# Performance work log

Measured on AMD Instinct MI355X. Metric: run time of the kernel, lower is better.

## Reference

```python
import jax, jax.numpy as jnp
import numpy as np

EPS = 1e-5
SLOPE = 0.1
R = 7  # num_relation

def _bn(x, g, b):
    # BatchNorm1d in training mode: per-feature batch mean / biased variance
    m = jnp.mean(x, axis=0)
    v = jnp.var(x, axis=0)
    return (x - m) * jax.lax.rsqrt(v + EPS) * g + b

def _lrelu(x):
    return jnp.where(x >= 0, x, SLOPE * x)

def setup_inputs() -> dict:
    key = jax.random.key(0)
    ks = jax.random.split(key, 10)
    N, E, D, DE = 50000, 800000, 128, 64
    h_v = jax.random.normal(ks[0], (N, D), dtype=jnp.float32)
    node_in = jax.random.randint(ks[1], (E,), 0, N)
    node_out = jax.random.randint(ks[2], (E,), 0, N)
    relation_type = jax.random.randint(ks[3], (E,), 0, R)
    h_e = jax.random.normal(ks[4], (E, DE), dtype=jnp.float32)
    s = 0.02
    return {
        "h_v": h_v, "node_in": node_in, "node_out": node_out,
        "relation_type": relation_type, "h_e": h_e,
        # input MLP: BN -> LReLU -> Linear(D,D,bias) -> BN -> LReLU
        "in_bn1_g": jnp.ones((D,)), "in_bn1_b": jnp.zeros((D,)),
        "in_W": jax.random.normal(ks[5], (D, D), dtype=jnp.float32) * s,
        "in_b": jnp.zeros((D,)),
        "in_bn2_g": jnp.ones((D,)), "in_bn2_b": jnp.zeros((D,)),
        # edge MLP: BN -> LReLU -> Linear(DE,D,bias) -> BN -> LReLU
        "e_bn1_g": jnp.ones((DE,)), "e_bn1_b": jnp.zeros((DE,)),
        "e_W": jax.random.normal(ks[6], (DE, D), dtype=jnp.float32) * s,
        "e_b": jnp.zeros((D,)),
        "e_bn2_g": jnp.ones((D,)), "e_bn2_b": jnp.zeros((D,)),
        # linear: BN(R*D) -> LReLU -> Linear(R*D, D, no bias)
        "lin_bn_g": jnp.ones((R * D,)), "lin_bn_b": jnp.zeros((R * D,)),
        "lin_W": jax.random.normal(ks[7], (R * D, D), dtype=jnp.float32) * s,
        # output: BN(D) -> LReLU -> Linear(D, D, no bias)
        "out_bn_g": jnp.ones((D,)), "out_bn_b": jnp.zeros((D,)),
        "out_W": jax.random.normal(ks[8], (D, D), dtype=jnp.float32) * s,
    }

def reference(h_v, node_in, node_out, relation_type, h_e,
              in_bn1_g, in_bn1_b, in_W, in_b, in_bn2_g, in_bn2_b,
              e_bn1_g, e_bn1_b, e_W, e_b, e_bn2_g, e_bn2_b,
              lin_bn_g, lin_bn_b, lin_W, out_bn_g, out_bn_b, out_W):
    N, D = h_v.shape
    identity = h_v  # input_dim == output_dim -> identity branch is passthrough
    # self.input MLP
    x = _lrelu(_bn(h_v, in_bn1_g, in_bn1_b))
    x = x @ in_W + in_b
    x = _lrelu(_bn(x, in_bn2_g, in_bn2_b))
    # gather + edge MLP add
    msg = x[node_in]  # [E, D]
    e = _lrelu(_bn(h_e, e_bn1_g, e_bn1_b))
    e = e @ e_W + e_b
    e = _lrelu(_bn(e, e_bn2_g, e_bn2_b))
    msg = msg + e
    # relation-indexed scatter_sum
    seg = node_out * R + relation_type  # [E]
    update = jax.ops.segment_sum(msg, seg, num_segments=N * R)  # [N*R, D]
    update = update.reshape(N, R * D)
    # self.linear
    out = _lrelu(_bn(update, lin_bn_g, lin_bn_b)) @ lin_W
    # self.output + residual
    out = _lrelu(_bn(out, out_bn_g, out_bn_b)) @ out_W + identity
    return out
```

## Files before the change

kernel.cpp:

```cpp
#include <hip/hip_runtime.h>

#define EPS 1e-5f
#define SLOPE 0.1f
#define DIM 128
#define DE 64
#define RNUM 7
#define RD (RNUM * DIM)
#define NPB 4

__device__ __forceinline__ float lrelu(float x) { return x >= 0.f ? x : SLOPE * x; }
__device__ __forceinline__ void atomAddF(float* p, float v) { unsafeAtomicAdd(p, v); }

template<int F, int BLK>
__global__ void colstats(const float* __restrict__ x, int nrows, float* __restrict__ out) {
  constexpr int G = BLK / F;
  int f = threadIdx.x % F;
  int g = threadIdx.x / F;
  float s = 0.f, q = 0.f;
  for (int r = blockIdx.x * G + g; r < nrows; r += gridDim.x * G) {
    float v = x[(size_t)r * F + f];
    s += v; q += v * v;
  }
  if constexpr (G > 1) {
    __shared__ float ls[BLK], lq[BLK];
    ls[threadIdx.x] = s; lq[threadIdx.x] = q;
    __syncthreads();
    if (g == 0) {
      #pragma unroll
      for (int i = 1; i < G; i++) { s += ls[i * F + f]; q += lq[i * F + f]; }
    }
  }
  if (g == 0) { atomAddF(&out[f], s); atomAddF(&out[F + f], q); }
}

template<bool HAS_BIAS, bool RESID, bool STATS>
__global__ __launch_bounds__(128) void mlp128(
    const float* __restrict__ xin, const float* __restrict__ W,
    const float* __restrict__ bias,
    const float* __restrict__ bng, const float* __restrict__ bnb,
    const float* __restrict__ stats_in, float invN, int N,
    const float* __restrict__ resid,
    float* __restrict__ out, float* __restrict__ stats_out) {
  __shared__ float tile[32 * DIM];
  int t = threadIdx.x;
  float a, c;
  {
    float mean = stats_in[t] * invN;
    float var = stats_in[DIM + t] * invN - mean * mean;
    a = bng[t] * rsqrtf(var + EPS);
    c = bnb[t] - mean * a;
  }
  int r0 = blockIdx.x * 32;
  int nr = min(32, N - r0);
  for (int r = 0; r < 32; r++) {
    float v = 0.f;
    if (r < nr) {
      v = xin[(size_t)(r0 + r) * DIM + t];
      v = lrelu(v * a + c);
    }
    tile[r * DIM + t] = v;
  }
  __syncthreads();
  int cg = t & 31, rg = t >> 5;
  float acc[8][4];
  #pragma unroll
  for (int rr = 0; rr < 8; rr++) { acc[rr][0]=0.f; acc[rr][1]=0.f; acc[rr][2]=0.f; acc[rr][3]=0.f; }
  const float4* W4 = (const float4*)W;
  #pragma unroll 2
  for (int k = 0; k < DIM; k += 4) {
    float4 w0 = W4[(k + 0) * 32 + cg];
    float4 w1 = W4[(k + 1) * 32 + cg];
    float4 w2 = W4[(k + 2) * 32 + cg];
    float4 w3 = W4[(k + 3) * 32 + cg];
    #pragma unroll
    for (int rr = 0; rr < 8; rr++) {
      float4 tv = *(const float4*)&tile[(rg * 8 + rr) * DIM + k];
      acc[rr][0] += tv.x * w0.x + tv.y * w1.x + tv.z * w2.x + tv.w * w3.x;
      acc[rr][1] += tv.x * w0.y + tv.y * w1.y + tv.z * w2.y + tv.w * w3.y;
      acc[rr][2] += tv.x * w0.z + tv.y * w1.z + tv.z * w2.z + tv.w * w3.z;
      acc[rr][3] += tv.x * w0.w + tv.y * w1.w + tv.z * w2.w + tv.w * w3.w;
    }
  }
  float4 bv = make_float4(0.f, 0.f, 0.f, 0.f);
  if (HAS_BIAS) bv = ((const float4*)bias)[cg];
  float s0=0,s1=0,s2=0,s3=0,q0=0,q1=0,q2=0,q3=0;
  #pragma unroll
  for (int rr = 0; rr < 8; rr++) {
    int r = rg * 8 + rr;
    if (r < nr) {
      float o0 = acc[rr][0] + bv.x;
      float o1 = acc[rr][1] + bv.y;
      float o2 = acc[rr][2] + bv.z;
      float o3 = acc[rr][3] + bv.w;
      if (RESID) {
        const float4 rv = *(const float4*)&resid[(size_t)(r0 + r) * DIM + cg * 4];
        o0 += rv.x; o1 += rv.y; o2 += rv.z; o3 += rv.w;
      }
      *(float4*)&out[(size_t)(r0 + r) * DIM + cg * 4] = make_float4(o0, o1, o2, o3);
      if (STATS) {
        s0 += o0; q0 += o0 * o0; s1 += o1; q1 += o1 * o1;
        s2 += o2; q2 += o2 * o2; s3 += o3; q3 += o3 * o3;
      }
    }
  }
  if (STATS) {
    __syncthreads();
    float* reds = tile;
    float* redq = tile + 512;
    int col = cg * 4;
    reds[rg * DIM + col + 0] = s0; reds[rg * DIM + col + 1] = s1;
    reds[rg * DIM + col + 2] = s2; reds[rg * DIM + col + 3] = s3;
    redq[rg * DIM + col + 0] = q0; redq[rg * DIM + col + 1] = q1;
    redq[rg * DIM + col + 2] = q2; redq[rg * DIM + col + 3] = q3;
    __syncthreads();
    if (rg == 0) {
      #pragma unroll
      for (int cc = 0; cc < 4; cc++) {
        int cl = col + cc;
        float ss = reds[cl] + reds[DIM + cl] + reds[2 * DIM + cl] + reds[3 * DIM + cl];
        float qq = redq[cl] + redq[DIM + cl] + redq[2 * DIM + cl] + redq[3 * DIM + cl];
        atomAddF(&stats_out[cl], ss);
        atomAddF(&stats_out[DIM + cl], qq);
      }
    }
  }
}

__global__ __launch_bounds__(256) void x2k(float* __restrict__ x1,
    const float* __restrict__ s_x1, const float* __restrict__ g,
    const float* __restrict__ b, float invN, int total4) {
  int i = blockIdx.x * 256 + threadIdx.x;
  if (i >= total4) return;
  int col = (i & 31) * 4;
  float4 v = ((float4*)x1)[i];
  float m0 = s_x1[col + 0] * invN, m1 = s_x1[col + 1] * invN;
  float m2 = s_x1[col + 2] * invN, m3 = s_x1[col + 3] * invN;
  float a0 = g[col + 0] * rsqrtf(s_x1[DIM + col + 0] * invN - m0 * m0 + EPS);
  float a1 = g[col + 1] * rsqrtf(s_x1[DIM + col + 1] * invN - m1 * m1 + EPS);
  float a2 = g[col + 2] * rsqrtf(s_x1[DIM + col + 2] * invN - m2 * m2 + EPS);
  float a3 = g[col + 3] * rsqrtf(s_x1[DIM + col + 3] * invN - m3 * m3 + EPS);
  v.x = lrelu(v.x * a0 + (b[col + 0] - m0 * a0));
  v.y = lrelu(v.y * a1 + (b[col + 1] - m1 * a1));
  v.z = lrelu(v.z * a2 + (b[col + 2] - m2 * a2));
  v.w = lrelu(v.w * a3 + (b[col + 3] - m3 * a3));
  ((float4*)x1)[i] = v;
}

__global__ __launch_bounds__(128) void lin_mlp(
    const float* __restrict__ upd, const float* __restrict__ W,
    const float* __restrict__ bng, const float* __restrict__ bnb,
    const float* __restrict__ stats_in, float invN, int N,
    float* __restrict__ out, float* __restrict__ stats_out) {
  __shared__ float tile[32 * DIM];
  int t = threadIdx.x;
  int r0 = blockIdx.x * 32;
  int nr = min(32, N - r0);
  int cg = t & 31, rg = t >> 5;
  float acc[8][4];
  #pragma unroll
  for (int rr = 0; rr < 8; rr++) { acc[rr][0]=0.f; acc[rr][1]=0.f; acc[rr][2]=0.f; acc[rr][3]=0.f; }
  const float4* W4 = (const float4*)W;
  for (int kt = 0; kt < RNUM; kt++) {
    int cb = kt * DIM;
    float a, c;
    {
      int col = cb + t;
      float mean = stats_in[col] * invN;
      float var = stats_in[RD + col] * invN - mean * mean;
      a = bng[col] * rsqrtf(var + EPS);
      c = bnb[col] - mean * a;
    }
    for (int r = 0; r < 32; r++) {
      float v = 0.f;
      if (r < nr) {
        v = upd[(size_t)(r0 + r) * RD + cb + t];
        v = lrelu(v * a + c);
      }
      tile[r * DIM + t] = v;
    }
    __syncthreads();
    #pragma unroll 2
    for (int k = 0; k < DIM; k += 4) {
      float4 w0 = W4[(cb + k + 0) * 32 + cg];
      float4 w1 = W4[(cb + k + 1) * 32 + cg];
      float4 w2 = W4[(cb + k + 2) * 32 + cg];
      float4 w3 = W4[(cb + k + 3) * 32 + cg];
      #pragma unroll
      for (int rr = 0; rr < 8; rr++) {
        float4 tv = *(const float4*)&tile[(rg * 8 + rr) * DIM + k];
        acc[rr][0] += tv.x * w0.x + tv.y * w1.x + tv.z * w2.x + tv.w * w3.x;
        acc[rr][1] += tv.x * w0.y + tv.y * w1.y + tv.z * w2.y + tv.w * w3.y;
        acc[rr][2] += tv.x * w0.z + tv.y * w1.z + tv.z * w2.z + tv.w * w3.z;
        acc[rr][3] += tv.x * w0.w + tv.y * w1.w + tv.z * w2.w + tv.w * w3.w;
      }
    }
    __syncthreads();
  }
  float s0=0,s1=0,s2=0,s3=0,q0=0,q1=0,q2=0,q3=0;
  #pragma unroll
  for (int rr = 0; rr < 8; rr++) {
    int r = rg * 8 + rr;
    if (r < nr) {
      float o0 = acc[rr][0], o1 = acc[rr][1], o2 = acc[rr][2], o3 = acc[rr][3];
      *(float4*)&out[(size_t)(r0 + r) * DIM + cg * 4] = make_float4(o0, o1, o2, o3);
      s0 += o0; q0 += o0 * o0; s1 += o1; q1 += o1 * o1;
      s2 += o2; q2 += o2 * o2; s3 += o3; q3 += o3 * o3;
    }
  }
  __syncthreads();
  float* reds = tile;
  float* redq = tile + 512;
  int col = cg * 4;
  reds[rg * DIM + col + 0] = s0; reds[rg * DIM + col + 1] = s1;
  reds[rg * DIM + col + 2] = s2; reds[rg * DIM + col + 3] = s3;
  redq[rg * DIM + col + 0] = q0; redq[rg * DIM + col + 1] = q1;
  redq[rg * DIM + col + 2] = q2; redq[rg * DIM + col + 3] = q3;
  __syncthreads();
  if (rg == 0) {
    #pragma unroll
    for (int cc = 0; cc < 4; cc++) {
      int cl = col + cc;
      float ss = reds[cl] + reds[DIM + cl] + reds[2 * DIM + cl] + reds[3 * DIM + cl];
      float qq = redq[cl] + redq[DIM + cl] + redq[2 * DIM + cl] + redq[3 * DIM + cl];
      atomAddF(&stats_out[cl], ss);
      atomAddF(&stats_out[DIM + cl], qq);
    }
  }
}

__global__ __launch_bounds__(256) void gram_kernel(
    const float* __restrict__ he, int E,
    const float* __restrict__ g1, const float* __restrict__ b1,
    const float* __restrict__ s_he, float invE,
    float* __restrict__ parts, int tilesPerBlock) {
  __shared__ float yt[32 * DE];
  int t = threadIdx.x;
  int f = t & 63;
  float a, c;
  {
    float mean = s_he[f] * invE;
    float var = s_he[DE + f] * invE - mean * mean;
    a = g1[f] * rsqrtf(var + EPS);
    c = b1[f] - mean * a;
  }
  int k1b = t >> 4, k2b = t & 15;
  float accG[4][4];
  #pragma unroll
  for (int i = 0; i < 4; i++) { accG[i][0]=0.f; accG[i][1]=0.f; accG[i][2]=0.f; accG[i][3]=0.f; }
  float colsum = 0.f;
  long long tile0 = (long long)blockIdx.x * tilesPerBlock;
  for (int tt = 0; tt < tilesPerBlock; tt++) {
    int e0 = (int)((tile0 + tt) * 32);
    if (e0 >= E) break;
    __syncthreads();
    #pragma unroll
    for (int i = 0; i < 8; i++) {
      int r = (t + i * 256) >> 6;
      int e = e0 + r;
      float v = 0.f;
      if (e < E) v = lrelu(he[(size_t)e * DE + f] * a + c);
      yt[r * DE + f] = v;
      colsum += v;
    }
    __syncthreads();
    #pragma unroll 4
    for (int r = 0; r < 32; r++) {
      float4 ya = *(const float4*)&yt[r * DE + k1b * 4];
      float4 yb = *(const float4*)&yt[r * DE + k2b * 4];
      accG[0][0] += ya.x * yb.x; accG[0][1] += ya.x * yb.y; accG[0][2] += ya.x * yb.z; accG[0][3] += ya.x * yb.w;
      accG[1][0] += ya.y * yb.x; accG[1][1] += ya.y * yb.y; accG[1][2] += ya.y * yb.z; accG[1][3] += ya.y * yb.w;
      accG[2][0] += ya.z * yb.x; accG[2][1] += ya.z * yb.y; accG[2][2] += ya.z * yb.z; accG[2][3] += ya.z * yb.w;
      accG[3][0] += ya.w * yb.x; accG[3][1] += ya.w * yb.y; accG[3][2] += ya.w * yb.z; accG[3][3] += ya.w * yb.w;
    }
  }
  __syncthreads();
  yt[t] = colsum;
  __syncthreads();
  float* outp = parts + (size_t)blockIdx.x * 4160;
  #pragma unroll
  for (int i = 0; i < 4; i++)
    #pragma unroll
    for (int j = 0; j < 4; j++)
      outp[(k1b * 4 + i) * DE + k2b * 4 + j] = accG[i][j];
  if (t < DE) outp[4096 + t] = yt[t] + yt[t + 64] + yt[t + 128] + yt[t + 192];
}

__global__ __launch_bounds__(256) void gram_reduce(const float* __restrict__ parts, int P,
    float* __restrict__ gram, float* __restrict__ gcol) {
  int j = blockIdx.x * 256 + threadIdx.x;
  if (j >= 4160) return;
  float s = 0.f;
  for (int p = 0; p < P; p++) s += parts[(size_t)p * 4160 + j];
  if (j < 4096) gram[j] = s; else gcol[j - 4096] = s;
}

__global__ __launch_bounds__(128) void ebn2_partial(
    const float* __restrict__ gram, const float* __restrict__ gcol,
    const float* __restrict__ eW, float invE,
    float* __restrict__ q, float* __restrict__ m1) {
  int j = threadIdx.x;
  int k1 = blockIdx.x;
  float wk1 = eW[k1 * DIM + j];
  float s = 0.f;
  for (int k2 = 0; k2 < DE; k2++) s += eW[k2 * DIM + j] * gram[k1 * DE + k2];
  atomAddF(&q[j], wk1 * s * invE);
  if (k1 == 0) {
    float m = 0.f;
    for (int k = 0; k < DE; k++) m += gcol[k] * eW[k * DIM + j];
    m1[j] = m * invE;
  }
}

__global__ void count_k(const int* __restrict__ nout, int E, int* __restrict__ cnt) {
  for (int e = blockIdx.x * blockDim.x + threadIdx.x; e < E; e += gridDim.x * blockDim.x)
    atomicAdd(&cnt[nout[e]], 1);
}

__global__ __launch_bounds__(256) void scan1(const int* __restrict__ in, int n,
    int* __restrict__ excl, int* __restrict__ sums) {
  __shared__ int s[256];
  int i = blockIdx.x * 256 + threadIdx.x;
  int v = (i < n) ? in[i] : 0;
  s[threadIdx.x] = v; __syncthreads();
  for (int off = 1; off < 256; off <<= 1) {
    int x = (threadIdx.x >= off) ? s[threadIdx.x - off] : 0;
    __syncthreads(); s[threadIdx.x] += x; __syncthreads();
  }
  if (i < n) excl[i] = s[threadIdx.x] - v;
  if (threadIdx.x == 255) sums[blockIdx.x] = s[255];
}

__global__ __launch_bounds__(1024) void scan2(int* __restrict__ sums, int nch) {
  __shared__ int s[1024];
  int t = threadIdx.x;
  int v = (t < nch) ? sums[t] : 0;
  s[t] = v; __syncthreads();
  for (int off = 1; off < 1024; off <<= 1) {
    int x = (t >= off) ? s[t - off] : 0;
    __syncthreads(); s[t] += x; __syncthreads();
  }
  if (t < nch) sums[t] = s[t] - v;
}

__global__ __launch_bounds__(256) void scan3(const int* __restrict__ excl,
    const int* __restrict__ sums, int n, int E,
    int* __restrict__ base, int* __restrict__ cursor) {
  int i = blockIdx.x * 256 + threadIdx.x;
  if (i < n) { int b = excl[i] + sums[blockIdx.x]; base[i] = b; cursor[i] = b; }
  if (i == 0) base[n] = E;
}

__global__ void scatter_k(const int* __restrict__ nout, const int* __restrict__ nin,
    const int* __restrict__ rel, int E, int* __restrict__ cursor, int2* __restrict__ elist2) {
  for (int e = blockIdx.x * blockDim.x + threadIdx.x; e < E; e += gridDim.x * blockDim.x) {
    int n = nout[e];
    int pos = atomicAdd(&cursor[n], 1);
    elist2[pos] = make_int2(e, (nin[e] << 3) | rel[e]);
  }
}

__global__ __launch_bounds__(128) void fused_edge_scatter(
    const float* __restrict__ he, const int2* __restrict__ elist2,
    const int* __restrict__ base, const float* __restrict__ eW,
    const float* __restrict__ eg1, const float* __restrict__ eb1,
    const float* __restrict__ s_he, float invE,
    const float* __restrict__ qv, const float* __restrict__ m1v,
    const float* __restrict__ eg2, const float* __restrict__ eb2,
    const float* __restrict__ x2, int N, float* __restrict__ upd) {
  __shared__ float accs[NPB * RD];
  __shared__ float yt[32 * DE];
  __shared__ float a2s[DIM], c2s[DIM];
  __shared__ int s_eid[32], s_nl[32], s_gr[32];
  int t = threadIdx.x;
  int n0 = blockIdx.x * NPB;
  int f = t & 63;
  float ae1, ce1;
  {
    float me = s_he[f] * invE;
    float ve = s_he[DE + f] * invE - me * me;
    ae1 = eg1[f] * rsqrtf(ve + EPS);
    ce1 = eb1[f] - me * ae1;
  }
  {
    float m = m1v[t];
    float a = eg2[t] * rsqrtf(qv[t] - m * m + EPS);
    a2s[t] = a;
    c2s[t] = eb2[t] - m * a;
  }
  for (int i = t; i < NPB * RD; i += 128) accs[i] = 0.f;
  int estart = base[n0];
  int eend = base[min(n0 + NPB, N)];
  int bb1 = base[min(n0 + 1, N)];
  int bb2 = base[min(n0 + 2, N)];
  int bb3 = base[min(n0 + 3, N)];
  __syncthreads();
  int cg = t & 31, rg = t >> 5;
  const float4* W4 = (const float4*)eW;
  for (int e0 = estart; e0 < eend; e0 += 32) {
    if (t < 32) {
      int pos = e0 + t;
      int2 ee = (pos < eend) ? elist2[pos] : make_int2(0, 0);
      s_eid[t] = ee.x;
      s_gr[t] = ee.y;
      s_nl[t] = (pos >= bb3) ? 3 : (pos >= bb2) ? 2 : (pos >= bb1) ? 1 : 0;
    }
    __syncthreads();
    #pragma unroll
    for (int i = 0; i < 16; i++) {
      int r = (t + i * 128) >> 6;
      float v = 0.f;
      if (e0 + r < eend) v = lrelu(he[(size_t)s_eid[r] * DE + f] * ae1 + ce1);
      yt[r * DE + f] = v;
    }
    __syncthreads();
    float a8[8][4];
    #pragma unroll
    for (int rr = 0; rr < 8; rr++) { a8[rr][0]=0.f; a8[rr][1]=0.f; a8[rr][2]=0.f; a8[rr][3]=0.f; }
    #pragma unroll 2
    for (int k = 0; k < DE; k += 4) {
      float4 w0 = W4[(k + 0) * 32 + cg];
      float4 w1 = W4[(k + 1) * 32 + cg];
      float4 w2 = W4[(k + 2) * 32 + cg];
      float4 w3 = W4[(k + 3) * 32 + cg];
      #pragma unroll
      for (int rr = 0; rr < 8; rr++) {
        float4 tv = *(const float4*)&yt[(rg * 8 + rr) * DE + k];
        a8[rr][0] += tv.x * w0.x + tv.y * w1.x + tv.z * w2.x + tv.w * w3.x;
        a8[rr][1] += tv.x * w0.y + tv.y * w1.y + tv.z * w2.y + tv.w * w3.y;
        a8[rr][2] += tv.x * w0.z + tv.y * w1.z + tv.z * w2.z + tv.w * w3.z;
        a8[rr][3] += tv.x * w0.w + tv.y * w1.w + tv.z * w2.w + tv.w * w3.w;
      }
    }
    float4 a2 = *(const float4*)&a2s[cg * 4];
    float4 c2 = *(const float4*)&c2s[cg * 4];
    int aoff[8];
    #pragma unroll
    for (int rr = 0; rr < 8; rr++) {
      int r = rg * 8 + rr;
      if (e0 + r < eend) {
        int gr = s_gr[r];
        const float4 xv = *(const float4*)&x2[(size_t)(gr >> 3) * DIM + cg * 4];
        a8[rr][0] = lrelu(a8[rr][0] * a2.x + c2.x) + xv.x;
        a8[rr][1] = lrelu(a8[rr][1] * a2.y + c2.y) + xv.y;
        a8[rr][2] = lrelu(a8[rr][2] * a2.z + c2.z) + xv.z;
        a8[rr][3] = lrelu(a8[rr][3] * a2.w + c2.w) + xv.w;
        aoff[rr] = s_nl[r] * RD + (gr & 7) * DIM + cg * 4;
      } else aoff[rr] = -1;
    }
    #pragma unroll
    for (int p = 0; p < 4; p++) {
      if (rg == p) {
        #pragma unroll
        for (int rr = 0; rr < 8; rr++) {
          int o = aoff[rr];
          if (o >= 0) {
            accs[o + 0] += a8[rr][0];
            accs[o + 1] += a8[rr][1];
            accs[o + 2] += a8[rr][2];
            accs[o + 3] += a8[rr][3];
          }
        }
      }
      __syncthreads();
    }
  }
  int nn = min(NPB, N - n0);
  for (int i = t; i < nn * RD; i += 128)
    upd[(size_t)n0 * RD + i] = accs[i];
}

extern "C" void kernel_launch(void* const* d_in, const int* in_sizes, int n_in,
                              void* d_out, int out_size, void* d_ws, size_t ws_size,
                              hipStream_t stream) {
  const float* h_v      = (const float*)d_in[0];
  const int*   node_in  = (const int*)d_in[1];
  const int*   node_out = (const int*)d_in[2];
  const int*   rel      = (const int*)d_in[3];
  const float* h_e      = (const float*)d_in[4];
  const float* in_bn1_g = (const float*)d_in[5];
  const float* in_bn1_b = (const float*)d_in[6];
  const float* in_W     = (const float*)d_in[7];
  const float* in_b     = (const float*)d_in[8];
  const float* in_bn2_g = (const float*)d_in[9];
  const float* in_bn2_b = (const float*)d_in[10];
  const float* e_bn1_g  = (const float*)d_in[11];
  const float* e_bn1_b  = (const float*)d_in[12];
  const float* e_W      = (const float*)d_in[13];
  const float* e_bn2_g  = (const float*)d_in[15];
  const float* e_bn2_b  = (const float*)d_in[16];
  const float* lin_bn_g = (const float*)d_in[17];
  const float* lin_bn_b = (const float*)d_in[18];
  const float* lin_W    = (const float*)d_in[19];
  const float* out_bn_g = (const float*)d_in[20];
  const float* out_bn_b = (const float*)d_in[21];
  const float* out_W    = (const float*)d_in[22];

  int N = in_sizes[0] / DIM;
  int E = in_sizes[1];
  if (N <= 0 || E <= 0) return;
  float invN = 1.f / (float)N;
  float invE = 1.f / (float)E;

  float* ws   = (float*)d_ws;
  float* upd  = ws;
  float* x1   = upd + (size_t)N * RD;
  float* stats = x1 + (size_t)N * DIM;
  float* s_hv = stats;
  float* s_x1 = s_hv + 2 * DIM;
  float* s_he = s_x1 + 2 * DIM;
  float* qv   = s_he + 2 * DE;
  float* m1v  = qv + DIM;
  float* s_up = m1v + DIM;
  float* s_o1 = s_up + 2 * RD;
  float* gram = s_o1 + 2 * DIM;
  float* gcol = gram + DE * DE;
  float* statsEnd = gcol + DE;
  size_t statsFloats = (size_t)(statsEnd - stats);
  int2* elist2 = (int2*)statsEnd;
  int* cnt    = (int*)(elist2 + E);
  int* sums   = cnt + N;
  int* base   = sums + 1024;
  int* cursor = base + N + 1;
  float* parts = upd;

  int nBlk32 = (N + 31) / 32;
  int nch = (N + 255) / 256;

  hipMemsetAsync(stats, 0, statsFloats * sizeof(float), stream);
  hipMemsetAsync(cnt, 0, (size_t)N * sizeof(int), stream);

  colstats<DIM, 256><<<512, 256, 0, stream>>>(h_v, N, s_hv);
  mlp128<true, false, true><<<nBlk32, 128, 0, stream>>>(
      h_v, in_W, in_b, in_bn1_g, in_bn1_b, s_hv, invN, N, nullptr, x1, s_x1);
  x2k<<<(N * 32 + 255) / 256, 256, 0, stream>>>(x1, s_x1, in_bn2_g, in_bn2_b, invN, N * 32);

  colstats<DE, 256><<<1024, 256, 0, stream>>>(h_e, E, s_he);

  count_k<<<1024, 256, 0, stream>>>(node_out, E, cnt);
  scan1<<<nch, 256, 0, stream>>>(cnt, N, cnt, sums);
  scan2<<<1, 1024, 0, stream>>>(sums, nch);
  scan3<<<nch, 256, 0, stream>>>(cnt, sums, N, E, base, cursor);
  scatter_k<<<1024, 256, 0, stream>>>(node_out, node_in, rel, E, cursor, elist2);

  {
    int tiles = 32;
    int P = (E + 32 * tiles - 1) / (32 * tiles);
    gram_kernel<<<P, 256, 0, stream>>>(h_e, E, e_bn1_g, e_bn1_b, s_he, invE, parts, tiles);
    gram_reduce<<<(4160 + 255) / 256, 256, 0, stream>>>(parts, P, gram, gcol);
  }
  ebn2_partial<<<DE, 128, 0, stream>>>(gram, gcol, e_W, invE, qv, m1v);

  fused_edge_scatter<<<(N + NPB - 1) / NPB, 128, 0, stream>>>(
      h_e, elist2, base, e_W, e_bn1_g, e_bn1_b, s_he, invE,
      qv, m1v, e_bn2_g, e_bn2_b, x1, N, upd);

  colstats<RD, RD><<<448, RD, 0, stream>>>(upd, N, s_up);
  lin_mlp<<<nBlk32, 128, 0, stream>>>(upd, lin_W, lin_bn_g, lin_bn_b, s_up, invN, N,
                                      x1, s_o1);
  mlp128<false, true, false><<<nBlk32, 128, 0, stream>>>(
      x1, out_W, nullptr, out_bn_g, out_bn_b, s_o1, invN, N, h_v, (float*)d_out, nullptr);
}
```

Measured before the change: 2.099 ms.

## Retile GEMM kernels to 4x8 register blocks and fold input BN into edge scatter

```diff
diff --git a/kernel.cpp b/kernel.cpp
--- a/kernel.cpp
+++ b/kernel.cpp
@@ -7,6 +7,8 @@
 #define RNUM 7
 #define RD (RNUM * DIM)
 #define NPB 4
+#define TP 132
+#define YP 68
 
 __device__ __forceinline__ float lrelu(float x) { return x >= 0.f ? x : SLOPE * x; }
 __device__ __forceinline__ void atomAddF(float* p, float v) { unsafeAtomicAdd(p, v); }
@@ -41,7 +43,7 @@
     const float* __restrict__ stats_in, float invN, int N,
     const float* __restrict__ resid,
     float* __restrict__ out, float* __restrict__ stats_out) {
-  __shared__ float tile[32 * DIM];
+  __shared__ float tile[32 * TP];
   int t = threadIdx.x;
   float a, c;
   {
@@ -58,92 +60,86 @@
       v = xin[(size_t)(r0 + r) * DIM + t];
       v = lrelu(v * a + c);
     }
-    tile[r * DIM + t] = v;
+    tile[r * TP + t] = v;
   }
   __syncthreads();
-  int cg = t & 31, rg = t >> 5;
-  float acc[8][4];
-  #pragma unroll
-  for (int rr = 0; rr < 8; rr++) { acc[rr][0]=0.f; acc[rr][1]=0.f; acc[rr][2]=0.f; acc[rr][3]=0.f; }
+  int cg = t & 15, rg = t >> 4;
+  int c0 = cg * 8;
+  float acc[4][8];
+  #pragma unroll
+  for (int rr = 0; rr < 4; rr++)
+    #pragma unroll
+    for (int j = 0; j < 8; j++) acc[rr][j] = 0.f;
   const float4* W4 = (const float4*)W;
   #pragma unroll 2
   for (int k = 0; k < DIM; k += 4) {
-    float4 w0 = W4[(k + 0) * 32 + cg];
-    float4 w1 = W4[(k + 1) * 32 + cg];
-    float4 w2 = W4[(k + 2) * 32 + cg];
-    float4 w3 = W4[(k + 3) * 32 + cg];
-    #pragma unroll
-    for (int rr = 0; rr < 8; rr++) {
-      float4 tv = *(const float4*)&tile[(rg * 8 + rr) * DIM + k];
-      acc[rr][0] += tv.x * w0.x + tv.y * w1.x + tv.z * w2.x + tv.w * w3.x;
-      acc[rr][1] += tv.x * w0.y + tv.y * w1.y + tv.z * w2.y + tv.w * w3.y;
-      acc[rr][2] += tv.x * w0.z + tv.y * w1.z + tv.z * w2.z + tv.w * w3.z;
-      acc[rr][3] += tv.x * w0.w + tv.y * w1.w + tv.z * w2.w + tv.w * w3.w;
-    }
-  }
-  float4 bv = make_float4(0.f, 0.f, 0.f, 0.f);
-  if (HAS_BIAS) bv = ((const float4*)bias)[cg];
-  float s0=0,s1=0,s2=0,s3=0,q0=0,q1=0,q2=0,q3=0;
-  #pragma unroll
-  for (int rr = 0; rr < 8; rr++) {
-    int r = rg * 8 + rr;
+    float4 wa0 = W4[(k + 0) * 32 + cg * 2], wb0 = W4[(k + 0) * 32 + cg * 2 + 1];
+    float4 wa1 = W4[(k + 1) * 32 + cg * 2], wb1 = W4[(k + 1) * 32 + cg * 2 + 1];
+    float4 wa2 = W4[(k + 2) * 32 + cg * 2], wb2 = W4[(k + 2) * 32 + cg * 2 + 1];
+    float4 wa3 = W4[(k + 3) * 32 + cg * 2], wb3 = W4[(k + 3) * 32 + cg * 2 + 1];
+    #pragma unroll
+    for (int rr = 0; rr < 4; rr++) {
+      float4 tv = *(const float4*)&tile[(rg * 4 + rr) * TP + k];
+      acc[rr][0] += tv.x * wa0.x + tv.y * wa1.x + tv.z * wa2.x + tv.w * wa3.x;
+      acc[rr][1] += tv.x * wa0.y + tv.y * wa1.y + tv.z * wa2.y + tv.w * wa3.y;
+      acc[rr][2] += tv.x * wa0.z + tv.y * wa1.z + tv.z * wa2.z + tv.w * wa3.z;
+      acc[rr][3] += tv.x * wa0.w + tv.y * wa1.w + tv.z * wa2.w + tv.w * wa3.w;
+      acc[rr][4] += tv.x * wb0.x + tv.y * wb1.x + tv.z * wb2.x + tv.w * wb3.x;
+      acc[rr][5] += tv.x * wb0.y + tv.y * wb1.y + tv.z * wb2.y + tv.w * wb3.y;
+      acc[rr][6] += tv.x * wb0.z + tv.y * wb1.z + tv.z * wb2.z + tv.w * wb3.z;
+      acc[rr][7] += tv.x * wb0.w + tv.y * wb1.w + tv.z * wb2.w + tv.w * wb3.w;
+    }
+  }
+  float bv[8];
+  #pragma unroll
+  for (int j = 0; j < 8; j++) bv[j] = 0.f;
+  if (HAS_BIAS) {
+    float4 ba = ((const float4*)bias)[cg * 2], bb = ((const float4*)bias)[cg * 2 + 1];
+    bv[0]=ba.x; bv[1]=ba.y; bv[2]=ba.z; bv[3]=ba.w; bv[4]=bb.x; bv[5]=bb.y; bv[6]=bb.z; bv[7]=bb.w;
+  }
+  float s[8], q[8];
+  #pragma unroll
+  for (int j = 0; j < 8; j++) { s[j] = 0.f; q[j] = 0.f; }
+  #pragma unroll
+  for (int rr = 0; rr < 4; rr++) {
+    int r = rg * 4 + rr;
     if (r < nr) {
-      float o0 = acc[rr][0] + bv.x;
-      float o1 = acc[rr][1] + bv.y;
-      float o2 = acc[rr][2] + bv.z;
-      float o3 = acc[rr][3] + bv.w;
+      float o[8];
+      #pragma unroll
+      for (int j = 0; j < 8; j++) o[j] = acc[rr][j] + bv[j];
       if (RESID) {
-        const float4 rv = *(const float4*)&resid[(size_t)(r0 + r) * DIM + cg * 4];
-        o0 += rv.x; o1 += rv.y; o2 += rv.z; o3 += rv.w;
-      }
-      *(float4*)&out[(size_t)(r0 + r) * DIM + cg * 4] = make_float4(o0, o1, o2, o3);
+        float4 ra = *(const float4*)&resid[(size_t)(r0 + r) * DIM + c0];
+        float4 rb = *(const float4*)&resid[(size_t)(r0 + r) * DIM + c0 + 4];
+        o[0]+=ra.x; o[1]+=ra.y; o[2]+=ra.z; o[3]+=ra.w;
+        o[4]+=rb.x; o[5]+=rb.y; o[6]+=rb.z; o[7]+=rb.w;
+      }
+      *(float4*)&out[(size_t)(r0 + r) * DIM + c0]     = make_float4(o[0], o[1], o[2], o[3]);
+      *(float4*)&out[(size_t)(r0 + r) * DIM + c0 + 4] = make_float4(o[4], o[5], o[6], o[7]);
       if (STATS) {
-        s0 += o0; q0 += o0 * o0; s1 += o1; q1 += o1 * o1;
-        s2 += o2; q2 += o2 * o2; s3 += o3; q3 += o3 * o3;
+        #pragma unroll
+        for (int j = 0; j < 8; j++) { s[j] += o[j]; q[j] += o[j] * o[j]; }
       }
     }
   }
   if (STATS) {
     __syncthreads();
     float* reds = tile;
-    float* redq = tile + 512;
-    int col = cg * 4;
-    reds[rg * DIM + col + 0] = s0; reds[rg * DIM + col + 1] = s1;
-    reds[rg * DIM + col + 2] = s2; reds[rg * DIM + col + 3] = s3;
-    redq[rg * DIM + col + 0] = q0; redq[rg * DIM + col + 1] = q1;
-    redq[rg * DIM + col + 2] = q2; redq[rg * DIM + col + 3] = q3;
+    float* redq = tile + 1024;
+    #pragma unroll
+    for (int j = 0; j < 8; j++) { reds[rg * DIM + c0 + j] = s[j]; redq[rg * DIM + c0 + j] = q[j]; }
     __syncthreads();
     if (rg == 0) {
       #pragma unroll
-      for (int cc = 0; cc < 4; cc++) {
-        int cl = col + cc;
-        float ss = reds[cl] + reds[DIM + cl] + reds[2 * DIM + cl] + reds[3 * DIM + cl];
-        float qq = redq[cl] + redq[DIM + cl] + redq[2 * DIM + cl] + redq[3 * DIM + cl];
+      for (int j = 0; j < 8; j++) {
+        int cl = c0 + j;
+        float ss = 0.f, qq = 0.f;
+        #pragma unroll
+        for (int g = 0; g < 8; g++) { ss += reds[g * DIM + cl]; qq += redq[g * DIM + cl]; }
         atomAddF(&stats_out[cl], ss);
         atomAddF(&stats_out[DIM + cl], qq);
       }
     }
   }
-}
-
-__global__ __launch_bounds__(256) void x2k(float* __restrict__ x1,
-    const float* __restrict__ s_x1, const float* __restrict__ g,
-    const float* __restrict__ b, float invN, int total4) {
-  int i = blockIdx.x * 256 + threadIdx.x;
-  if (i >= total4) return;
-  int col = (i & 31) * 4;
-  float4 v = ((float4*)x1)[i];
-  float m0 = s_x1[col + 0] * invN, m1 = s_x1[col + 1] * invN;
-  float m2 = s_x1[col + 2] * invN, m3 = s_x1[col + 3] * invN;
-  float a0 = g[col + 0] * rsqrtf(s_x1[DIM + col + 0] * invN - m0 * m0 + EPS);
-  float a1 = g[col + 1] * rsqrtf(s_x1[DIM + col + 1] * invN - m1 * m1 + EPS);
-  float a2 = g[col + 2] * rsqrtf(s_x1[DIM + col + 2] * invN - m2 * m2 + EPS);
-  float a3 = g[col + 3] * rsqrtf(s_x1[DIM + col + 3] * invN - m3 * m3 + EPS);
-  v.x = lrelu(v.x * a0 + (b[col + 0] - m0 * a0));
-  v.y = lrelu(v.y * a1 + (b[col + 1] - m1 * a1));
-  v.z = lrelu(v.z * a2 + (b[col + 2] - m2 * a2));
-  v.w = lrelu(v.w * a3 + (b[col + 3] - m3 * a3));
-  ((float4*)x1)[i] = v;
 }
 
 __global__ __launch_bounds__(128) void lin_mlp(
@@ -151,14 +147,17 @@
     const float* __restrict__ bng, const float* __restrict__ bnb,
     const float* __restrict__ stats_in, float invN, int N,
     float* __restrict__ out, float* __restrict__ stats_out) {
-  __shared__ float tile[32 * DIM];
+  __shared__ float tile[32 * TP];
   int t = threadIdx.x;
   int r0 = blockIdx.x * 32;
   int nr = min(32, N - r0);
-  int cg = t & 31, rg = t >> 5;
-  float acc[8][4];
-  #pragma unroll
-  for (int rr = 0; rr < 8; rr++) { acc[rr][0]=0.f; acc[rr][1]=0.f; acc[rr][2]=0.f; acc[rr][3]=0.f; }
+  int cg = t & 15, rg = t >> 4;
+  int c0 = cg * 8;
+  float acc[4][8];
+  #pragma unroll
+  for (int rr = 0; rr < 4; rr++)
+    #pragma unroll
+    for (int j = 0; j < 8; j++) acc[rr][j] = 0.f;
   const float4* W4 = (const float4*)W;
   for (int kt = 0; kt < RNUM; kt++) {
     int cb = kt * DIM;
@@ -176,52 +175,56 @@
         v = upd[(size_t)(r0 + r) * RD + cb + t];
         v = lrelu(v * a + c);
       }
-      tile[r * DIM + t] = v;
+      tile[r * TP + t] = v;
     }
     __syncthreads();
     #pragma unroll 2
     for (int k = 0; k < DIM; k += 4) {
-      float4 w0 = W4[(cb + k + 0) * 32 + cg];
-      float4 w1 = W4[(cb + k + 1) * 32 + cg];
-      float4 w2 = W4[(cb + k + 2) * 32 + cg];
-      float4 w3 = W4[(cb + k + 3) * 32 + cg];
-      #pragma unroll
-      for (int rr = 0; rr < 8; rr++) {
-        float4 tv = *(const float4*)&tile[(rg * 8 + rr) * DIM + k];
-        acc[rr][0] += tv.x * w0.x + tv.y * w1.x + tv.z * w2.x + tv.w * w3.x;
-        acc[rr][1] += tv.x * w0.y + tv.y * w1.y + tv.z * w2.y + tv.w * w3.y;
-        acc[rr][2] += tv.x * w0.z + tv.y * w1.z + tv.z * w2.z + tv.w * w3.z;
-        acc[rr][3] += tv.x * w0.w + tv.y * w1.w + tv.z * w2.w + tv.w * w3.w;
-      }
-    }
-    __syncthreads();
-  }
-  float s0=0,s1=0,s2=0,s3=0,q0=0,q1=0,q2=0,q3=0;
-  #pragma unroll
-  for (int rr = 0; rr < 8; rr++) {
-    int r = rg * 8 + rr;
+      float4 wa0 = W4[(cb + k + 0) * 32 + cg * 2], wb0 = W4[(cb + k + 0) * 32 + cg * 2 + 1];
+      float4 wa1 = W4[(cb + k + 1) * 32 + cg * 2], wb1 = W4[(cb + k + 1) * 32 + cg * 2 + 1];
+      float4 wa2 = W4[(cb + k + 2) * 32 + cg * 2], wb2 = W4[(cb + k + 2) * 32 + cg * 2 + 1];
+      float4 wa3 = W4[(cb + k + 3) * 32 + cg * 2], wb3 = W4[(cb + k + 3) * 32 + cg * 2 + 1];
+      #pragma unroll
+      for (int rr = 0; rr < 4; rr++) {
+        float4 tv = *(const float4*)&tile[(rg * 4 + rr) * TP + k];
+        acc[rr][0] += tv.x * wa0.x + tv.y * wa1.x + tv.z * wa2.x + tv.w * wa3.x;
+        acc[rr][1] += tv.x * wa0.y + tv.y * wa1.y + tv.z * wa2.y + tv.w * wa3.y;
+        acc[rr][2] += tv.x * wa0.z + tv.y * wa1.z + tv.z * wa2.z + tv.w * wa3.z;
+        acc[rr][3] += tv.x * wa0.w + tv.y * wa1.w + tv.z * wa2.w + tv.w * wa3.w;
+        acc[rr][4] += tv.x * wb0.x + tv.y * wb1.x + tv.z * wb2.x + tv.w * wb3.x;
+        acc[rr][5] += tv.x * wb0.y + tv.y * wb1.y + tv.z * wb2.y + tv.w * wb3.y;
+        acc[rr][6] += tv.x * wb0.z + tv.y * wb1.z + tv.z * wb2.z + tv.w * wb3.z;
+        acc[rr][7] += tv.x * wb0.w + tv.y * wb1.w + tv.z * wb2.w + tv.w * wb3.w;
+      }
+    }
+    __syncthreads();
+  }
+  float s[8], q[8];
+  #pragma unroll
+  for (int j = 0; j < 8; j++) { s[j] = 0.f; q[j] = 0.f; }
+  #pragma unroll
+  for (int rr = 0; rr < 4; rr++) {
+    int r = rg * 4 + rr;
     if (r < nr) {
-      float o0 = acc[rr][0], o1 = acc[rr][1], o2 = acc[rr][2], o3 = acc[rr][3];
-      *(float4*)&out[(size_t)(r0 + r) * DIM + cg * 4] = make_float4(o0, o1, o2, o3);
-      s0 += o0; q0 += o0 * o0; s1 += o1; q1 += o1 * o1;
-      s2 += o2; q2 += o2 * o2; s3 += o3; q3 += o3 * o3;
+      *(float4*)&out[(size_t)(r0 + r) * DIM + c0]     = make_float4(acc[rr][0], acc[rr][1], acc[rr][2], acc[rr][3]);
+      *(float4*)&out[(size_t)(r0 + r) * DIM + c0 + 4] = make_float4(acc[rr][4], acc[rr][5], acc[rr][6], acc[rr][7]);
+      #pragma unroll
+      for (int j = 0; j < 8; j++) { s[j] += acc[rr][j]; q[j] += acc[rr][j] * acc[rr][j]; }
     }
   }
   __syncthreads();
   float* reds = tile;
-  float* redq = tile + 512;
-  int col = cg * 4;
-  reds[rg * DIM + col + 0] = s0; reds[rg * DIM + col + 1] = s1;
-  reds[rg * DIM + col + 2] = s2; reds[rg * DIM + col + 3] = s3;
-  redq[rg * DIM + col + 0] = q0; redq[rg * DIM + col + 1] = q1;
-  redq[rg * DIM + col + 2] = q2; redq[rg * DIM + col + 3] = q3;
+  float* redq = tile + 1024;
+  #pragma unroll
+  for (int j = 0; j < 8; j++) { reds[rg * DIM + c0 + j] = s[j]; redq[rg * DIM + c0 + j] = q[j]; }
   __syncthreads();
   if (rg == 0) {
     #pragma unroll
-    for (int cc = 0; cc < 4; cc++) {
-      int cl = col + cc;
-      float ss = reds[cl] + reds[DIM + cl] + reds[2 * DIM + cl] + reds[3 * DIM + cl];
-      float qq = redq[cl] + redq[DIM + cl] + redq[2 * DIM + cl] + redq[3 * DIM + cl];
+    for (int j = 0; j < 8; j++) {
+      int cl = c0 + j;
+      float ss = 0.f, qq = 0.f;
+      #pragma unroll
+      for (int g = 0; g < 8; g++) { ss += reds[g * DIM + cl]; qq += redq[g * DIM + cl]; }
       atomAddF(&stats_out[cl], ss);
       atomAddF(&stats_out[DIM + cl], qq);
     }
@@ -366,13 +369,25 @@
     const float* __restrict__ s_he, float invE,
     const float* __restrict__ qv, const float* __restrict__ m1v,
     const float* __restrict__ eg2, const float* __restrict__ eb2,
-    const float* __restrict__ x2, int N, float* __restrict__ upd) {
+    const float* __restrict__ x1, const float* __restrict__ s_x1,
+    const float* __restrict__ ig2, const float* __restrict__ ib2, float invN,
+    int N, float* __restrict__ upd) {
   __shared__ float accs[NPB * RD];
-  __shared__ float yt[32 * DE];
-  __shared__ float a2s[DIM], c2s[DIM];
+  __shared__ float yt[32 * YP];
+  __shared__ float a2s[DIM], c2s[DIM], axs[DIM], cxs[DIM];
   __shared__ int s_eid[32], s_nl[32], s_gr[32];
   int t = threadIdx.x;
-  int n0 = blockIdx.x * NPB;
+  {
+    float m = m1v[t];
+    float aa = eg2[t] * rsqrtf(qv[t] - m * m + EPS);
+    a2s[t] = aa;
+    c2s[t] = eb2[t] - m * aa;
+    float mx = s_x1[t] * invN;
+    float vx = s_x1[DIM + t] * invN - mx * mx;
+    float ax = ig2[t] * rsqrtf(vx + EPS);
+    axs[t] = ax;
+    cxs[t] = ib2[t] - mx * ax;
+  }
   int f = t & 63;
   float ae1, ce1;
   {
@@ -381,22 +396,18 @@
     ae1 = eg1[f] * rsqrtf(ve + EPS);
     ce1 = eb1[f] - me * ae1;
   }
-  {
-    float m = m1v[t];
-    float a = eg2[t] * rsqrtf(qv[t] - m * m + EPS);
-    a2s[t] = a;
-    c2s[t] = eb2[t] - m * a;
-  }
   for (int i = t; i < NPB * RD; i += 128) accs[i] = 0.f;
+  int n0 = blockIdx.x * NPB;
   int estart = base[n0];
   int eend = base[min(n0 + NPB, N)];
   int bb1 = base[min(n0 + 1, N)];
   int bb2 = base[min(n0 + 2, N)];
   int bb3 = base[min(n0 + 3, N)];
-  __syncthreads();
-  int cg = t & 31, rg = t >> 5;
+  int cg = t & 15, rg = t >> 4;
+  int c0 = cg * 8;
   const float4* W4 = (const float4*)eW;
   for (int e0 = estart; e0 < eend; e0 += 32) {
+    __syncthreads();
     if (t < 32) {
       int pos = e0 + t;
       int2 ee = (pos < eend) ? elist2[pos] : make_int2(0, 0);
@@ -410,60 +421,60 @@
       int r = (t + i * 128) >> 6;
       float v = 0.f;
       if (e0 + r < eend) v = lrelu(he[(size_t)s_eid[r] * DE + f] * ae1 + ce1);
-      yt[r * DE + f] = v;
-    }
-    __syncthreads();
-    float a8[8][4];
-    #pragma unroll
-    for (int rr = 0; rr < 8; rr++) { a8[rr][0]=0.f; a8[rr][1]=0.f; a8[rr][2]=0.f; a8[rr][3]=0.f; }
+      yt[r * YP + f] = v;
+    }
+    __syncthreads();
+    float acc[4][8];
+    #pragma unroll
+    for (int rr = 0; rr < 4; rr++)
+      #pragma unroll
+      for (int j = 0; j < 8; j++) acc[rr][j] = 0.f;
     #pragma unroll 2
     for (int k = 0; k < DE; k += 4) {
-      float4 w0 = W4[(k + 0) * 32 + cg];
-      float4 w1 = W4[(k + 1) * 32 + cg];
-      float4 w2 = W4[(k + 2) * 32 + cg];
-      float4 w3 = W4[(k + 3) * 32 + cg];
-      #pragma unroll
-      for (int rr = 0; rr < 8; rr++) {
-        float4 tv = *(const float4*)&yt[(rg * 8 + rr) * DE + k];
-        a8[rr][0] += tv.x * w0.x + tv.y * w1.x + tv.z * w2.x + tv.w * w3.x;
-        a8[rr][1] += tv.x * w0.y + tv.y * w1.y + tv.z * w2.y + tv.w * w3.y;
-        a8[rr][2] += tv.x * w0.z + tv.y * w1.z + tv.z * w2.z + tv.w * w3.z;
-        a8[rr][3] += tv.x * w0.w + tv.y * w1.w + tv.z * w2.w + tv.w * w3.w;
-      }
-    }
-    float4 a2 = *(const float4*)&a2s[cg * 4];
-    float4 c2 = *(const float4*)&c2s[cg * 4];
-    int aoff[8];
-    #pragma unroll
-    for (int rr = 0; rr < 8; rr++) {
-      int r = rg * 8 + rr;
-      if (e0 + r < eend) {
-        int gr = s_gr[r];
-        const float4 xv = *(const float4*)&x2[(size_t)(gr >> 3) * DIM + cg * 4];
-        a8[rr][0] = lrelu(a8[rr][0] * a2.x + c2.x) + xv.x;
-        a8[rr][1] = lrelu(a8[rr][1] * a2.y + c2.y) + xv.y;
-        a8[rr][2] = lrelu(a8[rr][2] * a2.z + c2.z) + xv.z;
-        a8[rr][3] = lrelu(a8[rr][3] * a2.w + c2.w) + xv.w;
-        aoff[rr] = s_nl[r] * RD + (gr & 7) * DIM + cg * 4;
-      } else aoff[rr] = -1;
-    }
-    #pragma unroll
-    for (int p = 0; p < 4; p++) {
-      if (rg == p) {
-        #pragma unroll
-        for (int rr = 0; rr < 8; rr++) {
-          int o = aoff[rr];
-          if (o >= 0) {
-            accs[o + 0] += a8[rr][0];
-            accs[o + 1] += a8[rr][1];
-            accs[o + 2] += a8[rr][2];
-            accs[o + 3] += a8[rr][3];
-          }
+      float4 wa0 = W4[(k + 0) * 32 + cg * 2], wb0 = W4[(k + 0) * 32 + cg * 2 + 1];
+      float4 wa1 = W4[(k + 1) * 32 + cg * 2], wb1 = W4[(k + 1) * 32 + cg * 2 + 1];
+      float4 wa2 = W4[(k + 2) * 32 + cg * 2], wb2 = W4[(k + 2) * 32 + cg * 2 + 1];
+      float4 wa3 = W4[(k + 3) * 32 + cg * 2], wb3 = W4[(k + 3) * 32 + cg * 2 + 1];
+      #pragma unroll
+      for (int rr = 0; rr < 4; rr++) {
+        float4 tv = *(const float4*)&yt[(rg * 4 + rr) * YP + k];
+        acc[rr][0] += tv.x * wa0.x + tv.y * wa1.x + tv.z * wa2.x + tv.w * wa3.x;
+        acc[rr][1] += tv.x * wa0.y + tv.y * wa1.y + tv.z * wa2.y + tv.w * wa3.y;
+        acc[rr][2] += tv.x * wa0.z + tv.y * wa1.z + tv.z * wa2.z + tv.w * wa3.z;
+        acc[rr][3] += tv.x * wa0.w + tv.y * wa1.w + tv.z * wa2.w + tv.w * wa3.w;
+        acc[rr][4] += tv.x * wb0.x + tv.y * wb1.x + tv.z * wb2.x + tv.w * wb3.x;
+        acc[rr][5] += tv.x * wb0.y + tv.y * wb1.y + tv.z * wb2.y + tv.w * wb3.y;
+        acc[rr][6] += tv.x * wb0.z + tv.y * wb1.z + tv.z * wb2.z + tv.w * wb3.z;
+        acc[rr][7] += tv.x * wb0.w + tv.y * wb1.w + tv.z * wb2.w + tv.w * wb3.w;
+      }
+    }
+    {
+      float4 a2a = *(const float4*)&a2s[c0], a2b = *(const float4*)&a2s[c0 + 4];
+      float4 c2a = *(const float4*)&c2s[c0], c2b = *(const float4*)&c2s[c0 + 4];
+      float4 axa = *(const float4*)&axs[c0], axb = *(const float4*)&axs[c0 + 4];
+      float4 cxa = *(const float4*)&cxs[c0], cxb = *(const float4*)&cxs[c0 + 4];
+      #pragma unroll
+      for (int rr = 0; rr < 4; rr++) {
+        int r = rg * 4 + rr;
+        if (e0 + r < eend) {
+          int y = s_gr[r];
+          const float* xr = &x1[(size_t)(y >> 3) * DIM + c0];
+          float4 xva = *(const float4*)xr;
+          float4 xvb = *(const float4*)(xr + 4);
+          float* ap = &accs[s_nl[r] * RD + (y & 7) * DIM + c0];
+          atomicAdd(ap + 0, lrelu(acc[rr][0] * a2a.x + c2a.x) + lrelu(xva.x * axa.x + cxa.x));
+          atomicAdd(ap + 1, lrelu(acc[rr][1] * a2a.y + c2a.y) + lrelu(xva.y * axa.y + cxa.y));
+          atomicAdd(ap + 2, lrelu(acc[rr][2] * a2a.z + c2a.z) + lrelu(xva.z * axa.z + cxa.z));
+          atomicAdd(ap + 3, lrelu(acc[rr][3] * a2a.w + c2a.w) + lrelu(xva.w * axa.w + cxa.w));
+          atomicAdd(ap + 4, lrelu(acc[rr][4] * a2b.x + c2b.x) + lrelu(xvb.x * axb.x + cxb.x));
+          atomicAdd(ap + 5, lrelu(acc[rr][5] * a2b.y + c2b.y) + lrelu(xvb.y * axb.y + cxb.y));
+          atomicAdd(ap + 6, lrelu(acc[rr][6] * a2b.z + c2b.z) + lrelu(xvb.z * axb.z + cxb.z));
+          atomicAdd(ap + 7, lrelu(acc[rr][7] * a2b.w + c2b.w) + lrelu(xvb.w * axb.w + cxb.w));
         }
       }
-      __syncthreads();
-    }
-  }
+    }
+  }
+  __syncthreads();
   int nn = min(NPB, N - n0);
   for (int i = t; i < nn * RD; i += 128)
     upd[(size_t)n0 * RD + i] = accs[i];
@@ -532,7 +543,6 @@
   colstats<DIM, 256><<<512, 256, 0, stream>>>(h_v, N, s_hv);
   mlp128<true, false, true><<<nBlk32, 128, 0, stream>>>(
       h_v, in_W, in_b, in_bn1_g, in_bn1_b, s_hv, invN, N, nullptr, x1, s_x1);
-  x2k<<<(N * 32 + 255) / 256, 256, 0, stream>>>(x1, s_x1, in_bn2_g, in_bn2_b, invN, N * 32);
 
   colstats<DE, 256><<<1024, 256, 0, stream>>>(h_e, E, s_he);
 
@@ -552,7 +562,8 @@
 
   fused_edge_scatter<<<(N + NPB - 1) / NPB, 128, 0, stream>>>(
       h_e, elist2, base, e_W, e_bn1_g, e_bn1_b, s_he, invE,
-      qv, m1v, e_bn2_g, e_bn2_b, x1, N, upd);
+      qv, m1v, e_bn2_g, e_bn2_b, x1, s_x1, in_bn2_g, in_bn2_b, invN,
+      N, upd);
 
   colstats<RD, RD><<<448, RD, 0, stream>>>(upd, N, s_up);
   lin_mlp<<<nBlk32, 128, 0, stream>>>(upd, lin_W, lin_bn_g, lin_bn_b, s_up, invN, N,
```

After: 3.010 ms. 43.4% more time.
